# Kernel optimization log

Hardware: AMD Instinct MI355X
Metric: run time of the kernel (lower is better)

Reference implementation:

```python
import jax, jax.numpy as jnp
import numpy as np
from jax import lax

DN = ('NCDHW', 'OIDHW', 'NCDHW')


def dwconv(x, w, b):
    # depthwise 3D conv, 'same' padding (groups == channels of this branch)
    k = w.shape[-1]
    p = k // 2
    y = lax.conv_general_dilated(x, w, (1, 1, 1), [(p, p)] * 3,
                                 dimension_numbers=DN,
                                 feature_group_count=x.shape[1])
    return y + b[None, :, None, None, None]


def group_norm(x, w, b, groups=4, eps=1e-5):
    B, C, D, H, W = x.shape
    xr = x.reshape(B, groups, C // groups, D, H, W)
    mu = xr.mean(axis=(2, 3, 4, 5), keepdims=True)
    var = xr.var(axis=(2, 3, 4, 5), keepdims=True)
    xn = ((xr - mu) / jnp.sqrt(var + eps)).reshape(B, C, D, H, W)
    return xn * w[None, :, None, None, None] + b[None, :, None, None, None]


def instance_norm(x, eps=1e-5):
    # torch InstanceNorm3d default: affine=False, biased var, per (n,c) over spatial
    mu = x.mean(axis=(2, 3, 4), keepdims=True)
    var = x.var(axis=(2, 3, 4), keepdims=True)
    return (x - mu) / jnp.sqrt(var + eps)


def setup_inputs() -> dict:
    key = jax.random.key(0)
    B, C, D, H, W = 2, 32, 64, 64, 64
    gc = C // 4
    keys = jax.random.split(key, 12)
    inp = {"x": jax.random.normal(keys[0], (B, C, D, H, W), jnp.float32)}
    for i, k in enumerate([3, 5, 7, 9]):
        inp[f"w{k}"] = jax.random.normal(keys[1 + i], (gc, 1, k, k, k), jnp.float32) * (1.0 / k ** 1.5)
        inp[f"b{k}"] = jax.random.normal(keys[5 + i], (gc,), jnp.float32) * 0.01
    inp["gn_w"] = jnp.ones((C,), jnp.float32)
    inp["gn_b"] = jnp.zeros((C,), jnp.float32)
    inp["w_pw"] = jax.random.normal(keys[9], (gc, C), jnp.float32) * (1.0 / np.sqrt(C))
    inp["w_nxn"] = jax.random.normal(keys[10], (C, gc, 3, 3, 3), jnp.float32) * (1.0 / np.sqrt(gc * 27))
    return inp


def reference(x, w3, b3, w5, b5, w7, b7, w9, b9, gn_w, gn_b, w_pw, w_nxn):
    # split into 4 channel groups -> multi-kernel depthwise conv branches
    l, gs, gm, gl = jnp.split(x, 4, axis=1)
    y = jnp.concatenate([dwconv(l, w3, b3), dwconv(gs, w5, b5),
                         dwconv(gm, w7, b7), dwconv(gl, w9, b9)], axis=1) + x
    # GroupNorm(4) + exact GELU
    y = jax.nn.gelu(group_norm(y, gn_w, gn_b), approximate=False)
    # 1x1x1 conv (bias=False) + InstanceNorm + SiLU
    y = jax.nn.silu(instance_norm(jnp.einsum('bcdhw,oc->bodhw', y, w_pw)))
    # 3x3x3 conv (bias=False, pad 1) + InstanceNorm + SiLU
    y = lax.conv_general_dilated(y, w_nxn, (1, 1, 1), [(1, 1)] * 3, dimension_numbers=DN)
    y = jax.nn.silu(instance_norm(y))
    return y + x
```

## Files before the change

### kernel.cpp

```cpp
#include <hip/hip_runtime.h>
#include <cstddef>

#define SPATIAL (64*64*64)


__device__ __forceinline__ float wave_reduce(float v) {
    #pragma unroll
    for (int off = 32; off; off >>= 1) v += __shfl_down(v, off);
    return v;
}

__global__ void zero_stats(float* __restrict__ stats) {
    if (threadIdx.x < 176) stats[threadIdx.x] = 0.0f;
}


#define DW_RS   73
#define DW_SLICE (16 * DW_RS)
#define DW_RING 12

__device__ __forceinline__ void dw_stage(const float* __restrict__ xin,
                                         float* __restrict__ ring, int zd, int h0) {
    float* dst = ring + ((zd + 24) % DW_RING) * DW_SLICE;
    const float* src = xin + ((size_t)zd << 12);
    const bool dok = (unsigned)zd < 64u;
    for (int i = threadIdx.x; i < DW_SLICE; i += 256) {
        const int row = i / DW_RS;
        const int col = i - row * DW_RS;
        const int zh = h0 - 4 + row;
        const int zw = col - 4;
        float v = 0.0f;
        if (dok & ((unsigned)zh < 64u) & ((unsigned)zw < 64u)) v = src[(zh << 6) + zw];
        dst[i] = v;
    }
}

template<int K>
__device__ __forceinline__ void dw_impl(const float* __restrict__ x,
                                        const float* __restrict__ wsrc, float bias,
                                        int bc, int h0, int d0,
                                        float* __restrict__ ring,
                                        float* __restrict__ stats, int b,
                                        float* __restrict__ y1)
{
    constexpr int P = K / 2;
    constexpr int G = P - 1;
    constexpr int WIN = 8 + 2 * P;
    const float* xin = x + ((size_t)bc << 18);

    for (int zd = d0 - P; zd < d0 + P; ++zd) dw_stage(xin, ring, zd, h0);

    const int lane = threadIdx.x & 63;
    const int wave = threadIdx.x >> 6;
    const int w0   = (lane & 7) << 3;
    const int r    = lane >> 3;
    float gsum = 0.0f, gsq = 0.0f;

    for (int dq = d0; dq < d0 + 16; dq += 4) {
        #pragma unroll
        for (int j = 0; j < 4; ++j) dw_stage(xin, ring, dq + P + j, h0);
        __syncthreads();

        const int dd = dq + wave;
        float acc[8];
        #pragma unroll
        for (int i = 0; i < 8; ++i) acc[i] = bias;

        for (int kd = 0; kd < K; ++kd) {
            const float* sl = ring + ((dd + kd - P + 24) % DW_RING) * DW_SLICE;
            const float* wk = wsrc + kd * K * K;
            #pragma unroll
            for (int kh = 0; kh < K; ++kh) {
                const float* rowp = sl + (r + kh + 4 - P) * DW_RS + (w0 + 4 - P);
                float win[WIN];
                #pragma unroll
                for (int j = 0; j < WIN; ++j) win[j] = rowp[j];
                const float* wr = wk + kh * K;
                #pragma unroll
                for (int kw = 0; kw < K; ++kw) {
                    const float wt = wr[kw];
                    #pragma unroll
                    for (int i = 0; i < 8; ++i) acc[i] += win[kw + i] * wt;
                }
            }
        }
        const float* cen = ring + ((dd + 24) % DW_RING) * DW_SLICE + (r + 4) * DW_RS + (w0 + 4);
        #pragma unroll
        for (int i = 0; i < 8; ++i) acc[i] += cen[i];

        const size_t base = ((size_t)bc << 18) + ((size_t)dd << 12) +
                            ((size_t)(h0 + r) << 6) + w0;
        *(float4*)(y1 + base)     = make_float4(acc[0], acc[1], acc[2], acc[3]);
        *(float4*)(y1 + base + 4) = make_float4(acc[4], acc[5], acc[6], acc[7]);
        #pragma unroll
        for (int i = 0; i < 8; ++i) { gsum += acc[i]; gsq += acc[i] * acc[i]; }
        __syncthreads();
    }

    gsum = wave_reduce(gsum);
    gsq  = wave_reduce(gsq);
    if ((threadIdx.x & 63) == 0) {
        atomicAdd(&stats[b * 4 + G], gsum);
        atomicAdd(&stats[8 + b * 4 + G], gsq);
    }
}

__global__ __launch_bounds__(256) void dwconv_kernel(
    const float* __restrict__ x,
    const float* __restrict__ w3, const float* __restrict__ b3,
    const float* __restrict__ w5, const float* __restrict__ b5,
    const float* __restrict__ w7, const float* __restrict__ b7,
    const float* __restrict__ w9, const float* __restrict__ b9,
    float* __restrict__ y1, float* __restrict__ stats)
{
    __shared__ float ring[DW_RING * DW_SLICE];
    const int gid = blockIdx.x;
    const int g   = 3 - (gid >> 9);
    const int rr  = gid & 511;
    const int plane = rr >> 5;
    const int hq  = (rr >> 2) & 7;
    const int dc  = rr & 3;
    const int b   = plane >> 3, cl = plane & 7;
    const int bc  = (b << 5) + (g << 3) + cl;
    const int h0  = hq << 3, d0 = dc << 4;

    switch (g) {
        case 0: dw_impl<3>(x, w3 + cl * 27,  b3[cl], bc, h0, d0, ring, stats, b, y1); break;
        case 1: dw_impl<5>(x, w5 + cl * 125, b5[cl], bc, h0, d0, ring, stats, b, y1); break;
        case 2: dw_impl<7>(x, w7 + cl * 343, b7[cl], bc, h0, d0, ring, stats, b, y1); break;
        default: dw_impl<9>(x, w9 + cl * 729, b9[cl], bc, h0, d0, ring, stats, b, y1); break;
    }
}

__global__ void gn_finalize(const float* __restrict__ gn_w, const float* __restrict__ gn_b,
                            float* __restrict__ stats)
{
    const int i = threadIdx.x;
    if (i >= 64) return;
    const int b = i >> 5, c = i & 31, g = c >> 3;
    const float N = 8.0f * (float)SPATIAL;
    const float mu  = stats[b * 4 + g] / N;
    const float var = stats[8 + b * 4 + g] / N - mu * mu;
    const float rs  = rsqrtf(var + 1e-5f);
    const float a   = gn_w[c] * rs;
    stats[176 + i] = a;
    stats[240 + i] = gn_b[c] - mu * a;
}

__global__ __launch_bounds__(256) void pw_kernel(
    const float* __restrict__ y1, const float* __restrict__ w_pw,
    float* __restrict__ t, float* __restrict__ stats)
{
    const int bid = blockIdx.x;
    const int b   = bid >> 8;
    const int s   = (bid & 255) * 1024 + threadIdx.x * 4;

    const float* yb = y1 + ((size_t)b << 23);
    float acc[8][4] = {};

    for (int cc = 0; cc < 32; cc += 8) {
        float4 yv[8];
        #pragma unroll
        for (int u = 0; u < 8; ++u)
            yv[u] = *(const float4*)(yb + ((size_t)(cc + u) << 18) + s);
        #pragma unroll
        for (int u = 0; u < 8; ++u) {
            const int c = cc + u;
            const float ga = stats[176 + b * 32 + c];
            const float gs = stats[240 + b * 32 + c];
            float v0 = ga * yv[u].x + gs, v1 = ga * yv[u].y + gs;
            float v2 = ga * yv[u].z + gs, v3 = ga * yv[u].w + gs;
            const float e0 = 0.5f * v0 * (1.0f + erff(v0 * 0.70710678118654752f));
            const float e1 = 0.5f * v1 * (1.0f + erff(v1 * 0.70710678118654752f));
            const float e2 = 0.5f * v2 * (1.0f + erff(v2 * 0.70710678118654752f));
            const float e3 = 0.5f * v3 * (1.0f + erff(v3 * 0.70710678118654752f));
            #pragma unroll
            for (int o = 0; o < 8; ++o) {
                const float wt = w_pw[o * 32 + c];
                acc[o][0] += e0 * wt; acc[o][1] += e1 * wt;
                acc[o][2] += e2 * wt; acc[o][3] += e3 * wt;
            }
        }
    }

    float* tb = t + ((size_t)b << 21);
    #pragma unroll
    for (int o = 0; o < 8; ++o) {
        *(float4*)(tb + ((size_t)o << 18) + s) =
            make_float4(acc[o][0], acc[o][1], acc[o][2], acc[o][3]);
        float sm = acc[o][0] + acc[o][1] + acc[o][2] + acc[o][3];
        float sq = acc[o][0]*acc[o][0] + acc[o][1]*acc[o][1] +
                   acc[o][2]*acc[o][2] + acc[o][3]*acc[o][3];
        sm = wave_reduce(sm);
        sq = wave_reduce(sq);
        if ((threadIdx.x & 63) == 0) {
            atomicAdd(&stats[16 + b * 8 + o], sm);
            atomicAdd(&stats[32 + b * 8 + o], sq);
        }
    }
}

__global__ void in2_finalize(float* __restrict__ stats)
{
    const int i = threadIdx.x;
    if (i >= 16) return;
    const float N = (float)SPATIAL;
    const float mu  = stats[16 + i] / N;
    const float var = stats[32 + i] / N - mu * mu;
    stats[304 + i] = mu;
    stats[320 + i] = rsqrtf(var + 1e-5f);
}

#define C3_RS 41
#define C3_ROWSZ (10 * C3_RS)
#define C3_CH (3 * C3_ROWSZ)

__device__ __forceinline__ void c3_stage(const float* __restrict__ tb,
                                         float* __restrict__ ls,
                                         const float* __restrict__ stats,
                                         int b, int zd, int h0, int w0g)
{
    const bool dok = (unsigned)zd < 64u;
    const int slot = (zd + 33) % 3;
    for (int i = threadIdx.x; i < 8 * C3_ROWSZ; i += 256) {
        const int c   = i / C3_ROWSZ;
        const int rem = i - c * C3_ROWSZ;
        const int row = rem / C3_RS;
        const int col = rem - row * C3_RS;
        const int zh  = h0 - 1 + row;
        const int zw  = w0g + col - 4;
        float v = 0.0f;
        if (dok & ((unsigned)zh < 64u) & ((unsigned)zw < 64u)) {
            const float raw = tb[((size_t)c << 18) + ((size_t)zd << 12) + (zh << 6) + zw];
            const float mu = stats[304 + (b << 3) + c];
            const float rs = stats[320 + (b << 3) + c];
            const float xn = (raw - mu) * rs;
            v = xn / (1.0f + expf(-xn));
        }
        ls[c * C3_CH + slot * C3_ROWSZ + row * C3_RS + col] = v;
    }
}

__global__ __launch_bounds__(256) void conv3_kernel(
    const float* __restrict__ t, const float* __restrict__ w_nxn,
    float* __restrict__ out, float* __restrict__ stats)
{
    __shared__ float ls[8 * C3_CH];
    const int bid = blockIdx.x;
    const int b   = bid >> 8;
    const int r8  = bid & 255;
    const int d0  = (r8 >> 4) << 2;
    const int h0  = ((r8 >> 1) & 7) << 3;
    const int w0g = (r8 & 1) << 5;

    const int tid = threadIdx.x;
    const int w0  = (tid & 7) << 2;
    const int r   = (tid >> 3) & 7;
    const int oq  = __builtin_amdgcn_readfirstlane(tid >> 6);
    const int o0  = oq << 3;

    const float* tb = t + ((size_t)b << 21);
    float s3[8] = {}, q3[8] = {};

    c3_stage(tb, ls, stats, b, d0 - 1, h0, w0g);
    c3_stage(tb, ls, stats, b, d0,     h0, w0g);

    for (int d = d0; d < d0 + 4; ++d) {
        c3_stage(tb, ls, stats, b, d + 1, h0, w0g);
        __syncthreads();

        float acc[8][4] = {};
        for (int c = 0; c < 8; ++c) {
            const float* lc = ls + c * C3_CH;
            const float* wc = w_nxn + c * 27;
            #pragma unroll
            for (int kd = 0; kd < 3; ++kd) {
                const float* sl = lc + ((d + kd + 32) % 3) * C3_ROWSZ;
                #pragma unroll
                for (int kh = 0; kh < 3; ++kh) {
                    const float* rowp = sl + (r + kh) * C3_RS + w0 + 3;
                    float win[6];
                    #pragma unroll
                    for (int j = 0; j < 6; ++j) win[j] = rowp[j];
                    #pragma unroll
                    for (int oi = 0; oi < 8; ++oi) {
                        const float* wp = wc + (o0 + oi) * 216 + kd * 9 + kh * 3;
                        #pragma unroll
                        for (int kw = 0; kw < 3; ++kw) {
                            const float wt = wp[kw];
                            acc[oi][0] += win[kw]     * wt;
                            acc[oi][1] += win[kw + 1] * wt;
                            acc[oi][2] += win[kw + 2] * wt;
                            acc[oi][3] += win[kw + 3] * wt;
                        }
                    }
                }
            }
        }

        #pragma unroll
        for (int oi = 0; oi < 8; ++oi) {
            const int o = o0 + oi;
            *(float4*)(out + ((size_t)((b << 5) + o) << 18) + ((size_t)d << 12) +
                       ((size_t)(h0 + r) << 6) + (w0g + w0)) =
                make_float4(acc[oi][0], acc[oi][1], acc[oi][2], acc[oi][3]);
            s3[oi] += acc[oi][0] + acc[oi][1] + acc[oi][2] + acc[oi][3];
            q3[oi] += acc[oi][0]*acc[oi][0] + acc[oi][1]*acc[oi][1] +
                      acc[oi][2]*acc[oi][2] + acc[oi][3]*acc[oi][3];
        }
        __syncthreads();
    }

    #pragma unroll
    for (int oi = 0; oi < 8; ++oi) {
        float sm = wave_reduce(s3[oi]);
        float sq = wave_reduce(q3[oi]);
        if ((tid & 63) == 0) {
            atomicAdd(&stats[48 + (b << 5) + o0 + oi], sm);
            atomicAdd(&stats[112 + (b << 5) + o0 + oi], sq);
        }
    }
}

__global__ void in3_finalize(float* __restrict__ stats)
{
    const int i = threadIdx.x;
    if (i >= 64) return;
    const float N = (float)SPATIAL;
    const float mu  = stats[48 + i] / N;
    const float var = stats[112 + i] / N - mu * mu;
    stats[336 + i] = mu;
    stats[400 + i] = rsqrtf(var + 1e-5f);
}

__global__ __launch_bounds__(256) void final_kernel(
    const float* __restrict__ x, float* __restrict__ out, const float* __restrict__ stats)
{
    const int idx = blockIdx.x * 256 + threadIdx.x;
    const size_t i4 = (size_t)idx << 2;
    const int bc = (int)(i4 >> 18);
    const float mu = stats[336 + bc], rs = stats[400 + bc];
    float4 v = *(const float4*)(out + i4);
    const float4 xr = *(const float4*)(x + i4);
    v.x = (v.x - mu) * rs; v.x = v.x / (1.0f + expf(-v.x)) + xr.x;
    v.y = (v.y - mu) * rs; v.y = v.y / (1.0f + expf(-v.y)) + xr.y;
    v.z = (v.z - mu) * rs; v.z = v.z / (1.0f + expf(-v.z)) + xr.z;
    v.w = (v.w - mu) * rs; v.w = v.w / (1.0f + expf(-v.w)) + xr.w;
    *(float4*)(out + i4) = v;
}

extern "C" void kernel_launch(void* const* d_in, const int* in_sizes, int n_in,
                              void* d_out, int out_size, void* d_ws, size_t ws_size,
                              hipStream_t stream)
{
    const float* x    = (const float*)d_in[0];
    const float* w3   = (const float*)d_in[1];
    const float* b3   = (const float*)d_in[2];
    const float* w5   = (const float*)d_in[3];
    const float* b5   = (const float*)d_in[4];
    const float* w7   = (const float*)d_in[5];
    const float* b7   = (const float*)d_in[6];
    const float* w9   = (const float*)d_in[7];
    const float* b9   = (const float*)d_in[8];
    const float* gn_w = (const float*)d_in[9];
    const float* gn_b = (const float*)d_in[10];
    const float* w_pw = (const float*)d_in[11];
    const float* w_nxn= (const float*)d_in[12];

    char* ws = (char*)d_ws;
    float* t     = (float*)ws;
    float* stats = (float*)(ws + 16777216);

    float* out = (float*)d_out;

    zero_stats<<<1, 256, 0, stream>>>(stats);
    dwconv_kernel<<<2048, 256, 0, stream>>>(x, w3, b3, w5, b5, w7, b7, w9, b9, out, stats);
    gn_finalize<<<1, 64, 0, stream>>>(gn_w, gn_b, stats);
    pw_kernel<<<512, 256, 0, stream>>>(out, w_pw, t, stats);
    in2_finalize<<<1, 16, 0, stream>>>(stats);
    conv3_kernel<<<512, 256, 0, stream>>>(t, w_nxn, out, stats);
    in3_finalize<<<1, 64, 0, stream>>>(stats);
    final_kernel<<<16384, 256, 0, stream>>>(x, out, stats);
}
```

Before: 1.035 ms.

## Restructure depthwise conv tiles to reuse each loaded row across four depth outputs

```diff
diff --git a/kernel.cpp b/kernel.cpp
--- a/kernel.cpp
+++ b/kernel.cpp
@@ -15,91 +15,90 @@
 }
 
 
-#define DW_RS   73
+#define DW_RS    41
 #define DW_SLICE (16 * DW_RS)
-#define DW_RING 12
-
-__device__ __forceinline__ void dw_stage(const float* __restrict__ xin,
-                                         float* __restrict__ ring, int zd, int h0) {
-    float* dst = ring + ((zd + 24) % DW_RING) * DW_SLICE;
-    const float* src = xin + ((size_t)zd << 12);
-    const bool dok = (unsigned)zd < 64u;
-    for (int i = threadIdx.x; i < DW_SLICE; i += 256) {
-        const int row = i / DW_RS;
-        const int col = i - row * DW_RS;
-        const int zh = h0 - 4 + row;
-        const int zw = col - 4;
-        float v = 0.0f;
-        if (dok & ((unsigned)zh < 64u) & ((unsigned)zw < 64u)) v = src[(zh << 6) + zw];
-        dst[i] = v;
-    }
-}
 
 template<int K>
 __device__ __forceinline__ void dw_impl(const float* __restrict__ x,
                                         const float* __restrict__ wsrc, float bias,
-                                        int bc, int h0, int d0,
-                                        float* __restrict__ ring,
+                                        int bc, int h0, int d0, int w0g,
+                                        float* __restrict__ ls,
                                         float* __restrict__ stats, int b,
                                         float* __restrict__ y1)
 {
-    constexpr int P = K / 2;
-    constexpr int G = P - 1;
-    constexpr int WIN = 8 + 2 * P;
+    constexpr int P   = K / 2;
+    constexpr int G   = P - 1;
+    constexpr int WIN = 4 + 2 * P;
+    constexpr int NS  = 16 + 2 * P;
     const float* xin = x + ((size_t)bc << 18);
 
-    for (int zd = d0 - P; zd < d0 + P; ++zd) dw_stage(xin, ring, zd, h0);
+    for (int i = threadIdx.x; i < NS * 640; i += 256) {
+        const int zi  = i / 640;
+        const int rem = i - zi * 640;
+        const int row = rem / 40;
+        const int col = rem - row * 40;
+        const int zd = d0 - P + zi;
+        const int zh = h0 - 4 + row;
+        const int zw = w0g - 4 + col;
+        float v = 0.0f;
+        if (((unsigned)zd < 64u) & ((unsigned)zh < 64u) & ((unsigned)zw < 64u))
+            v = xin[((size_t)zd << 12) + (zh << 6) + zw];
+        ls[(zi + 4 - P) * DW_SLICE + row * DW_RS + col] = v;
+    }
+    __syncthreads();
 
     const int lane = threadIdx.x & 63;
     const int wave = threadIdx.x >> 6;
-    const int w0   = (lane & 7) << 3;
+    const int wl   = lane & 7;
     const int r    = lane >> 3;
-    float gsum = 0.0f, gsq = 0.0f;
-
-    for (int dq = d0; dq < d0 + 16; dq += 4) {
-        #pragma unroll
-        for (int j = 0; j < 4; ++j) dw_stage(xin, ring, dq + P + j, h0);
-        __syncthreads();
-
-        const int dd = dq + wave;
-        float acc[8];
-        #pragma unroll
-        for (int i = 0; i < 8; ++i) acc[i] = bias;
-
-        for (int kd = 0; kd < K; ++kd) {
-            const float* sl = ring + ((dd + kd - P + 24) % DW_RING) * DW_SLICE;
-            const float* wk = wsrc + kd * K * K;
+    const int dq   = d0 + (wave << 2);
+    const int s0   = (wave << 2) + 4 - P;
+
+    float acc[4][4];
+    #pragma unroll
+    for (int j = 0; j < 4; ++j)
+        #pragma unroll
+        for (int i = 0; i < 4; ++i) acc[j][i] = bias;
+
+    for (int zq = 0; zq < K + 3; ++zq) {
+        const float* sl = ls + (s0 + zq) * DW_SLICE;
+        for (int kh = 0; kh < K; ++kh) {
+            const float* rowp = sl + (r + kh + 4 - P) * DW_RS + ((wl << 2) + 4 - P);
+            float win[WIN];
             #pragma unroll
-            for (int kh = 0; kh < K; ++kh) {
-                const float* rowp = sl + (r + kh + 4 - P) * DW_RS + (w0 + 4 - P);
-                float win[WIN];
-                #pragma unroll
-                for (int j = 0; j < WIN; ++j) win[j] = rowp[j];
-                const float* wr = wk + kh * K;
-                #pragma unroll
-                for (int kw = 0; kw < K; ++kw) {
-                    const float wt = wr[kw];
+            for (int t = 0; t < WIN; ++t) win[t] = rowp[t];
+            #pragma unroll
+            for (int j = 0; j < 4; ++j) {
+                const int kd = zq - j;
+                if (kd >= 0 && kd < K) {
+                    const float* wr = wsrc + (kd * K + kh) * K;
                     #pragma unroll
-                    for (int i = 0; i < 8; ++i) acc[i] += win[kw + i] * wt;
+                    for (int kw = 0; kw < K; ++kw) {
+                        const float wt = wr[kw];
+                        #pragma unroll
+                        for (int i = 0; i < 4; ++i) acc[j][i] += win[kw + i] * wt;
+                    }
                 }
             }
         }
-        const float* cen = ring + ((dd + 24) % DW_RING) * DW_SLICE + (r + 4) * DW_RS + (w0 + 4);
-        #pragma unroll
-        for (int i = 0; i < 8; ++i) acc[i] += cen[i];
-
-        const size_t base = ((size_t)bc << 18) + ((size_t)dd << 12) +
-                            ((size_t)(h0 + r) << 6) + w0;
-        *(float4*)(y1 + base)     = make_float4(acc[0], acc[1], acc[2], acc[3]);
-        *(float4*)(y1 + base + 4) = make_float4(acc[4], acc[5], acc[6], acc[7]);
-        #pragma unroll
-        for (int i = 0; i < 8; ++i) { gsum += acc[i]; gsq += acc[i] * acc[i]; }
-        __syncthreads();
+    }
+
+    float gsum = 0.0f, gsq = 0.0f;
+    #pragma unroll
+    for (int j = 0; j < 4; ++j) {
+        const float* cen = ls + ((wave << 2) + 4 + j) * DW_SLICE + (r + 4) * DW_RS + 4 + (wl << 2);
+        #pragma unroll
+        for (int i = 0; i < 4; ++i) acc[j][i] += cen[i];
+        const size_t base = ((size_t)bc << 18) + ((size_t)(dq + j) << 12) +
+                            ((size_t)(h0 + r) << 6) + (w0g + (wl << 2));
+        *(float4*)(y1 + base) = make_float4(acc[j][0], acc[j][1], acc[j][2], acc[j][3]);
+        #pragma unroll
+        for (int i = 0; i < 4; ++i) { gsum += acc[j][i]; gsq += acc[j][i] * acc[j][i]; }
     }
 
     gsum = wave_reduce(gsum);
     gsq  = wave_reduce(gsq);
-    if ((threadIdx.x & 63) == 0) {
+    if (lane == 0) {
         atomicAdd(&stats[b * 4 + G], gsum);
         atomicAdd(&stats[8 + b * 4 + G], gsq);
     }
@@ -113,22 +112,24 @@
     const float* __restrict__ w9, const float* __restrict__ b9,
     float* __restrict__ y1, float* __restrict__ stats)
 {
-    __shared__ float ring[DW_RING * DW_SLICE];
+    __shared__ float ls[24 * DW_SLICE];
     const int gid = blockIdx.x;
-    const int g   = 3 - (gid >> 9);
-    const int rr  = gid & 511;
-    const int plane = rr >> 5;
-    const int hq  = (rr >> 2) & 7;
-    const int dc  = rr & 3;
+    const int g   = 3 - (gid >> 10);
+    const int rr  = gid & 1023;
+    const int plane = rr >> 6;
+    const int sub = rr & 63;
+    const int hq  = sub >> 3;
+    const int dc  = (sub >> 1) & 3;
+    const int wc  = sub & 1;
     const int b   = plane >> 3, cl = plane & 7;
     const int bc  = (b << 5) + (g << 3) + cl;
-    const int h0  = hq << 3, d0 = dc << 4;
+    const int h0  = hq << 3, d0 = dc << 4, w0g = wc << 5;
 
     switch (g) {
-        case 0: dw_impl<3>(x, w3 + cl * 27,  b3[cl], bc, h0, d0, ring, stats, b, y1); break;
-        case 1: dw_impl<5>(x, w5 + cl * 125, b5[cl], bc, h0, d0, ring, stats, b, y1); break;
-        case 2: dw_impl<7>(x, w7 + cl * 343, b7[cl], bc, h0, d0, ring, stats, b, y1); break;
-        default: dw_impl<9>(x, w9 + cl * 729, b9[cl], bc, h0, d0, ring, stats, b, y1); break;
+        case 0: dw_impl<3>(x, w3 + cl * 27,  b3[cl], bc, h0, d0, w0g, ls, stats, b, y1); break;
+        case 1: dw_impl<5>(x, w5 + cl * 125, b5[cl], bc, h0, d0, w0g, ls, stats, b, y1); break;
+        case 2: dw_impl<7>(x, w7 + cl * 343, b7[cl], bc, h0, d0, w0g, ls, stats, b, y1); break;
+        default: dw_impl<9>(x, w9 + cl * 729, b9[cl], bc, h0, d0, w0g, ls, stats, b, y1); break;
     }
 }
 
@@ -374,7 +375,7 @@
     float* out = (float*)d_out;
 
     zero_stats<<<1, 256, 0, stream>>>(stats);
-    dwconv_kernel<<<2048, 256, 0, stream>>>(x, w3, b3, w5, b5, w7, b7, w9, b9, out, stats);
+    dwconv_kernel<<<4096, 256, 0, stream>>>(x, w3, b3, w5, b5, w7, b7, w9, b9, out, stats);
     gn_finalize<<<1, 64, 0, stream>>>(gn_w, gn_b, stats);
     pw_kernel<<<512, 256, 0, stream>>>(out, w_pw, t, stats);
     in2_finalize<<<1, 16, 0, stream>>>(stats);
```

Result: slower. 1.192 ms (+15.1%).
